# Kernel optimization log

Measured on AMD Instinct MI355X. Metric: run time of the kernel, lower is better.

The kernel has to match this reference:

```python
import jax, jax.numpy as jnp
import numpy as np

N_NODES = 100000
N_EDGES = 1600000
D_IN = 128
D_OUT = 128
EPS = 1e-12  # torch F.normalize default eps


def setup_inputs() -> dict:
    key = jax.random.key(0)
    k1, k2, k3, k4, k5 = jax.random.split(key, 5)
    features = jax.random.normal(k1, (N_NODES, D_IN), dtype=jnp.float32)
    edge_src = jax.random.randint(k2, (N_EDGES,), 0, N_NODES, dtype=jnp.int64)
    edge_dst = jax.random.randint(k3, (N_EDGES,), 0, N_NODES, dtype=jnp.int64)
    node_mask = jnp.ones((N_NODES,), dtype=bool)
    W = jax.random.normal(k4, (D_OUT, D_IN), dtype=jnp.float32) * (1.0 / np.sqrt(D_IN))
    b = jax.random.normal(k5, (D_OUT,), dtype=jnp.float32) * 0.01
    return {"features": features, "edge_src": edge_src, "edge_dst": edge_dst,
            "node_mask": node_mask, "W": W, "b": b}


def reference(features, edge_src, edge_dst, node_mask, W, b):
    # Message passing: sum neighbor (src) features into each dst node.
    msgs = features[edge_src]                                   # [E, D_IN]
    agg = jax.ops.segment_sum(msgs, edge_dst, num_segments=features.shape[0])  # [N, D_IN]
    # Active nodes: h_N[node] = features[node] + sum(neighbors); inactive keep features.
    h_N = jnp.where(node_mask[:, None], features + agg, features)
    # F.normalize(h_N, dim=1): L2 normalize rows with eps clamp.
    norm = jnp.linalg.norm(h_N, axis=1, keepdims=True)
    h_norm = h_N / jnp.maximum(norm, EPS)
    # Linear layer.
    return h_norm @ W.T + b
```

## Files before the change

kernel.cpp:

```cpp
#include <hip/hip_runtime.h>

#define N_NODES 100000
#define D 128
#define N_EDGES 1600000
#define NBINS 391
#define BCAP 8192
#define EPB 4000
#define AST 136
#define LCAP 64

typedef unsigned short u16;
typedef __attribute__((ext_vector_type(8))) short short8;
typedef __attribute__((ext_vector_type(8))) unsigned short ushort8;
typedef __attribute__((ext_vector_type(4))) float f32x4;

__device__ __forceinline__ u16 f2bf(float f) {
    union { float f; unsigned int i; } c;
    c.f = f;
    unsigned int r = c.i + 0x7FFFu + ((c.i >> 16) & 1u);
    return (u16)(r >> 16);
}

__device__ __forceinline__ void bf16_acc8(unsigned int u, float* a) {
    union { unsigned int i; float f; } c;
    c.i = u << 16;          a[0] += c.f;
    c.i = u & 0xffff0000u;  a[1] += c.f;
}

__global__ __launch_bounds__(256) void conv_all(const float* __restrict__ feat,
                                                const float* __restrict__ Wg,
                                                u16* __restrict__ featb,
                                                u16* __restrict__ Wbf,
                                                int* __restrict__ gcnt) {
    const int b = blockIdx.x, t = threadIdx.x;
    if (b < 6250) {
        if (!featb) return;
        int idx = (b * 256 + t) * 8;
        f32x4 v0 = *(const f32x4*)(feat + idx);
        f32x4 v1 = *(const f32x4*)(feat + idx + 4);
        ushort8 o;
        o[0] = f2bf(v0.x); o[1] = f2bf(v0.y); o[2] = f2bf(v0.z); o[3] = f2bf(v0.w);
        o[4] = f2bf(v1.x); o[5] = f2bf(v1.y); o[6] = f2bf(v1.z); o[7] = f2bf(v1.w);
        *(ushort8*)(featb + idx) = o;
    } else if (b < 6258) {
        int idx = ((b - 6250) * 256 + t) * 8;
        f32x4 v0 = *(const f32x4*)(Wg + idx);
        f32x4 v1 = *(const f32x4*)(Wg + idx + 4);
        ushort8 o;
        o[0] = f2bf(v0.x); o[1] = f2bf(v0.y); o[2] = f2bf(v0.z); o[3] = f2bf(v0.w);
        o[4] = f2bf(v1.x); o[5] = f2bf(v1.y); o[6] = f2bf(v1.z); o[7] = f2bf(v1.w);
        *(ushort8*)(Wbf + idx) = o;
    } else {
        gcnt[t] = 0;
        gcnt[t + 256] = 0;
    }
}

__global__ __launch_bounds__(256) void bin_edges(const int* __restrict__ esrc,
                                                 const int* __restrict__ edst,
                                                 int* __restrict__ gcnt,
                                                 unsigned* __restrict__ pool) {
    __shared__ unsigned stash[EPB];
    __shared__ u16 sbin[EPB];
    __shared__ int hist[NBINS];
    __shared__ int hbase[NBINS];
    const int t = threadIdx.x;
    const int base = blockIdx.x * EPB;

    for (int bb = t; bb < NBINS; bb += 256) hist[bb] = 0;
    __syncthreads();
    for (int i = t; i < EPB; i += 256) {
        int s = esrc[base + i];
        int d0 = edst[base + i];
        stash[i] = ((unsigned)(d0 & 255) << 17) | (unsigned)s;
        sbin[i] = (u16)(d0 >> 8);
        atomicAdd(&hist[d0 >> 8], 1);
    }
    __syncthreads();
    for (int bb = t; bb < NBINS; bb += 256) {
        int h = hist[bb];
        hbase[bb] = h ? atomicAdd(gcnt + bb, h) : 0;
        hist[bb] = 0;
    }
    __syncthreads();
    for (int i = t; i < EPB; i += 256) {
        int bb = sbin[i];
        int r  = atomicAdd(&hist[bb], 1);
        int pos = hbase[bb] + r;
        if (pos < BCAP) pool[bb * BCAP + pos] = stash[i];
    }
}

template<bool BF16FEAT>
__global__ __launch_bounds__(256) void fused_gnl(const void* __restrict__ featv,
                                                 const int* __restrict__ gcnt,
                                                 const unsigned* __restrict__ pool,
                                                 const u16* __restrict__ Wbf,
                                                 const float* __restrict__ bg,
                                                 float* __restrict__ out) {
    __shared__ u16 Al[32 * AST];
    __shared__ int lists[32 * LCAP];
    __shared__ int lcnt[32];
    const int t = threadIdx.x;
    const int nbase = blockIdx.x * 32;
    const int nl = t >> 3;
    const int g = t & 7;
    const int n = nbase + nl;

    {
        const int bin = blockIdx.x >> 3;
        const unsigned sub = (unsigned)(blockIdx.x & 7) << 5;
        int ne = gcnt[bin];
        if (ne > BCAP) ne = BCAP;
        if (t < 32) lcnt[t] = 0;
        __syncthreads();
        const unsigned* seg = pool + bin * BCAP;
        for (int i = t; i < ne; i += 256) {
            unsigned p = seg[i];
            unsigned rel = (p >> 17) - sub;
            if (rel < 32u) {
                int r = atomicAdd(&lcnt[rel], 1);
                if (r < LCAP) lists[rel * LCAP + r] = (int)(p & 0x1FFFFu);
            }
        }
        __syncthreads();
    }

    float acc[16];
    if (BF16FEAT) {
        const u16* fb = (const u16*)featv + (size_t)n * D + g * 16;
        uint4 p0 = *(const uint4*)(fb);
        uint4 p1 = *(const uint4*)(fb + 8);
        #pragma unroll
        for (int k = 0; k < 16; k++) acc[k] = 0.f;
        bf16_acc8(p0.x, acc + 0);  bf16_acc8(p0.y, acc + 2);
        bf16_acc8(p0.z, acc + 4);  bf16_acc8(p0.w, acc + 6);
        bf16_acc8(p1.x, acc + 8);  bf16_acc8(p1.y, acc + 10);
        bf16_acc8(p1.z, acc + 12); bf16_acc8(p1.w, acc + 14);
    } else {
        const float* ff = (const float*)featv + (size_t)n * D + g * 16;
        f32x4 v0 = *(const f32x4*)(ff);
        f32x4 v1 = *(const f32x4*)(ff + 4);
        f32x4 v2 = *(const f32x4*)(ff + 8);
        f32x4 v3 = *(const f32x4*)(ff + 12);
        acc[0]=v0.x; acc[1]=v0.y; acc[2]=v0.z; acc[3]=v0.w;
        acc[4]=v1.x; acc[5]=v1.y; acc[6]=v1.z; acc[7]=v1.w;
        acc[8]=v2.x; acc[9]=v2.y; acc[10]=v2.z; acc[11]=v2.w;
        acc[12]=v3.x; acc[13]=v3.y; acc[14]=v3.z; acc[15]=v3.w;
    }

    int deg = lcnt[nl];
    if (deg > LCAP) deg = LCAP;
    const int* bk = lists + nl * LCAP;
    int e = 0;
    if (BF16FEAT) {
        const u16* fb = (const u16*)featv;
        for (; e + 4 <= deg; e += 4) {
            int4 s4 = *(const int4*)(bk + e);
            const u16* r0 = fb + (size_t)s4.x * D + g * 16;
            const u16* r1 = fb + (size_t)s4.y * D + g * 16;
            const u16* r2 = fb + (size_t)s4.z * D + g * 16;
            const u16* r3 = fb + (size_t)s4.w * D + g * 16;
            uint4 a0 = *(const uint4*)(r0), b0 = *(const uint4*)(r0 + 8);
            uint4 a1 = *(const uint4*)(r1), b1 = *(const uint4*)(r1 + 8);
            uint4 a2 = *(const uint4*)(r2), b2 = *(const uint4*)(r2 + 8);
            uint4 a3 = *(const uint4*)(r3), b3 = *(const uint4*)(r3 + 8);
            bf16_acc8(a0.x, acc+0); bf16_acc8(a0.y, acc+2); bf16_acc8(a0.z, acc+4); bf16_acc8(a0.w, acc+6);
            bf16_acc8(b0.x, acc+8); bf16_acc8(b0.y, acc+10); bf16_acc8(b0.z, acc+12); bf16_acc8(b0.w, acc+14);
            bf16_acc8(a1.x, acc+0); bf16_acc8(a1.y, acc+2); bf16_acc8(a1.z, acc+4); bf16_acc8(a1.w, acc+6);
            bf16_acc8(b1.x, acc+8); bf16_acc8(b1.y, acc+10); bf16_acc8(b1.z, acc+12); bf16_acc8(b1.w, acc+14);
            bf16_acc8(a2.x, acc+0); bf16_acc8(a2.y, acc+2); bf16_acc8(a2.z, acc+4); bf16_acc8(a2.w, acc+6);
            bf16_acc8(b2.x, acc+8); bf16_acc8(b2.y, acc+10); bf16_acc8(b2.z, acc+12); bf16_acc8(b2.w, acc+14);
            bf16_acc8(a3.x, acc+0); bf16_acc8(a3.y, acc+2); bf16_acc8(a3.z, acc+4); bf16_acc8(a3.w, acc+6);
            bf16_acc8(b3.x, acc+8); bf16_acc8(b3.y, acc+10); bf16_acc8(b3.z, acc+12); bf16_acc8(b3.w, acc+14);
        }
        for (; e < deg; e++) {
            const u16* r0 = fb + (size_t)bk[e] * D + g * 16;
            uint4 a0 = *(const uint4*)(r0), b0 = *(const uint4*)(r0 + 8);
            bf16_acc8(a0.x, acc+0); bf16_acc8(a0.y, acc+2); bf16_acc8(a0.z, acc+4); bf16_acc8(a0.w, acc+6);
            bf16_acc8(b0.x, acc+8); bf16_acc8(b0.y, acc+10); bf16_acc8(b0.z, acc+12); bf16_acc8(b0.w, acc+14);
        }
    } else {
        const float* ff = (const float*)featv;
        for (; e + 2 <= deg; e += 2) {
            int2 s2 = *(const int2*)(bk + e);
            const float* r0 = ff + (size_t)s2.x * D + g * 16;
            const float* r1 = ff + (size_t)s2.y * D + g * 16;
            f32x4 x0 = *(const f32x4*)(r0),     x1 = *(const f32x4*)(r0 + 4);
            f32x4 x2 = *(const f32x4*)(r0 + 8), x3 = *(const f32x4*)(r0 + 12);
            f32x4 y0 = *(const f32x4*)(r1),     y1 = *(const f32x4*)(r1 + 4);
            f32x4 y2 = *(const f32x4*)(r1 + 8), y3 = *(const f32x4*)(r1 + 12);
            acc[0]+=x0.x+y0.x; acc[1]+=x0.y+y0.y; acc[2]+=x0.z+y0.z; acc[3]+=x0.w+y0.w;
            acc[4]+=x1.x+y1.x; acc[5]+=x1.y+y1.y; acc[6]+=x1.z+y1.z; acc[7]+=x1.w+y1.w;
            acc[8]+=x2.x+y2.x; acc[9]+=x2.y+y2.y; acc[10]+=x2.z+y2.z; acc[11]+=x2.w+y2.w;
            acc[12]+=x3.x+y3.x; acc[13]+=x3.y+y3.y; acc[14]+=x3.z+y3.z; acc[15]+=x3.w+y3.w;
        }
        for (; e < deg; e++) {
            const float* r0 = ff + (size_t)bk[e] * D + g * 16;
            f32x4 x0 = *(const f32x4*)(r0),     x1 = *(const f32x4*)(r0 + 4);
            f32x4 x2 = *(const f32x4*)(r0 + 8), x3 = *(const f32x4*)(r0 + 12);
            acc[0]+=x0.x; acc[1]+=x0.y; acc[2]+=x0.z; acc[3]+=x0.w;
            acc[4]+=x1.x; acc[5]+=x1.y; acc[6]+=x1.z; acc[7]+=x1.w;
            acc[8]+=x2.x; acc[9]+=x2.y; acc[10]+=x2.z; acc[11]+=x2.w;
            acc[12]+=x3.x; acc[13]+=x3.y; acc[14]+=x3.z; acc[15]+=x3.w;
        }
    }

    float ss = 0.f;
    #pragma unroll
    for (int k = 0; k < 16; k++) ss += acc[k] * acc[k];
    #pragma unroll
    for (int off = 4; off; off >>= 1) ss += __shfl_xor(ss, off, 8);
    const float inv = 1.0f / fmaxf(sqrtf(ss), 1e-12f);

    {
        ushort8 o0, o1;
        o0[0]=f2bf(acc[0]*inv); o0[1]=f2bf(acc[1]*inv); o0[2]=f2bf(acc[2]*inv); o0[3]=f2bf(acc[3]*inv);
        o0[4]=f2bf(acc[4]*inv); o0[5]=f2bf(acc[5]*inv); o0[6]=f2bf(acc[6]*inv); o0[7]=f2bf(acc[7]*inv);
        o1[0]=f2bf(acc[8]*inv); o1[1]=f2bf(acc[9]*inv); o1[2]=f2bf(acc[10]*inv); o1[3]=f2bf(acc[11]*inv);
        o1[4]=f2bf(acc[12]*inv); o1[5]=f2bf(acc[13]*inv); o1[6]=f2bf(acc[14]*inv); o1[7]=f2bf(acc[15]*inv);
        u16* dst = Al + nl * AST + g * 16;
        *(ushort8*)(dst)     = o0;
        *(ushort8*)(dst + 8) = o1;
    }
    __syncthreads();

    const int w = t >> 6, lane = t & 63;
    const int mb = (w >> 1) * 16, nb = (w & 1) * 64;
    const int quad = lane >> 4, r = lane & 15;
    f32x4 c0 = {0,0,0,0}, c1 = {0,0,0,0}, c2 = {0,0,0,0}, c3 = {0,0,0,0};
    #pragma unroll
    for (int kt = 0; kt < 4; kt++) {
        const int ko = kt * 32 + quad * 8;
        short8 a  = *(const short8*)(Al + (mb + r) * AST + ko);
        short8 b0 = *(const short8*)(Wbf + (nb +  0 + r) * D + ko);
        short8 b1 = *(const short8*)(Wbf + (nb + 16 + r) * D + ko);
        short8 b2 = *(const short8*)(Wbf + (nb + 32 + r) * D + ko);
        short8 b3 = *(const short8*)(Wbf + (nb + 48 + r) * D + ko);
        c0 = __builtin_amdgcn_mfma_f32_16x16x32_bf16(a, b0, c0, 0, 0, 0);
        c1 = __builtin_amdgcn_mfma_f32_16x16x32_bf16(a, b1, c1, 0, 0, 0);
        c2 = __builtin_amdgcn_mfma_f32_16x16x32_bf16(a, b2, c2, 0, 0, 0);
        c3 = __builtin_amdgcn_mfma_f32_16x16x32_bf16(a, b3, c3, 0, 0, 0);
    }

    {
        const float bb0 = bg[nb + r], bb1 = bg[nb + 16 + r];
        const float bb2 = bg[nb + 32 + r], bb3 = bg[nb + 48 + r];
        float* outb = out + (size_t)(nbase + mb + quad * 4) * D;
        #pragma unroll
        for (int reg = 0; reg < 4; reg++) {
            float* rowp = outb + reg * D + nb + r;
            rowp[0]  = c0[reg] + bb0;
            rowp[16] = c1[reg] + bb1;
            rowp[32] = c2[reg] + bb2;
            rowp[48] = c3[reg] + bb3;
        }
    }
}

__global__ __launch_bounds__(256) void scatter(const float* __restrict__ feat,
                                               const int* __restrict__ esrc,
                                               const int* __restrict__ edst,
                                               float* __restrict__ agg) {
    int gid = blockIdx.x * 256 + threadIdx.x;
    int e = gid >> 5;
    int q = (gid & 31) << 2;
    int s = esrc[e];
    int d0 = edst[e];
    const float4 a = *(const float4*)(feat + s * D + q);
    float* dst = agg + d0 * D + q;
    unsafeAtomicAdd(dst + 0, a.x);
    unsafeAtomicAdd(dst + 1, a.y);
    unsafeAtomicAdd(dst + 2, a.z);
    unsafeAtomicAdd(dst + 3, a.w);
}

__global__ __launch_bounds__(256) void norm_linear_mfma(const float* __restrict__ Wg,
                                                        const float* __restrict__ bg,
                                                        float* __restrict__ out) {
    __shared__ u16 Wl[128 * AST];
    __shared__ u16 Al[32 * AST];
    __shared__ float bl[128];
    const int t = threadIdx.x;
    const int nbase = blockIdx.x * 32;

    for (int idx = t * 8; idx < 128 * 128; idx += 256 * 8) {
        int row = idx >> 7, col = idx & 127;
        f32x4 v0 = *(const f32x4*)(Wg + idx);
        f32x4 v1 = *(const f32x4*)(Wg + idx + 4);
        u16* dst = Wl + row * AST + col;
        dst[0] = f2bf(v0.x); dst[1] = f2bf(v0.y); dst[2] = f2bf(v0.z); dst[3] = f2bf(v0.w);
        dst[4] = f2bf(v1.x); dst[5] = f2bf(v1.y); dst[6] = f2bf(v1.z); dst[7] = f2bf(v1.w);
    }
    if (t < 128) bl[t] = bg[t];
    {
        const int n = t >> 3, seg = t & 7;
        const float* src = out + (nbase + n) * D + seg * 16;
        f32x4 v0 = *(const f32x4*)(src);
        f32x4 v1 = *(const f32x4*)(src + 4);
        f32x4 v2 = *(const f32x4*)(src + 8);
        f32x4 v3 = *(const f32x4*)(src + 12);
        float ss = v0.x*v0.x + v0.y*v0.y + v0.z*v0.z + v0.w*v0.w
                 + v1.x*v1.x + v1.y*v1.y + v1.z*v1.z + v1.w*v1.w
                 + v2.x*v2.x + v2.y*v2.y + v2.z*v2.z + v2.w*v2.w
                 + v3.x*v3.x + v3.y*v3.y + v3.z*v3.z + v3.w*v3.w;
        #pragma unroll
        for (int off = 4; off; off >>= 1) ss += __shfl_xor(ss, off, 8);
        const float inv = 1.0f / fmaxf(sqrtf(ss), 1e-12f);
        u16* dst = Al + n * AST + seg * 16;
        dst[0]  = f2bf(v0.x * inv); dst[1]  = f2bf(v0.y * inv);
        dst[2]  = f2bf(v0.z * inv); dst[3]  = f2bf(v0.w * inv);
        dst[4]  = f2bf(v1.x * inv); dst[5]  = f2bf(v1.y * inv);
        dst[6]  = f2bf(v1.z * inv); dst[7]  = f2bf(v1.w * inv);
        dst[8]  = f2bf(v2.x * inv); dst[9]  = f2bf(v2.y * inv);
        dst[10] = f2bf(v2.z * inv); dst[11] = f2bf(v2.w * inv);
        dst[12] = f2bf(v3.x * inv); dst[13] = f2bf(v3.y * inv);
        dst[14] = f2bf(v3.z * inv); dst[15] = f2bf(v3.w * inv);
    }
    __syncthreads();

    const int w = t >> 6, lane = t & 63;
    const int mb = (w >> 1) * 16, nb = (w & 1) * 64;
    const int quad = lane >> 4, r = lane & 15;
    f32x4 c0 = {0,0,0,0}, c1 = {0,0,0,0}, c2 = {0,0,0,0}, c3 = {0,0,0,0};
    #pragma unroll
    for (int kt = 0; kt < 4; kt++) {
        const int ko = kt * 32 + quad * 8;
        short8 a = *(const short8*)(Al + (mb + r) * AST + ko);
        short8 b0 = *(const short8*)(Wl + (nb +  0 + r) * AST + ko);
        short8 b1 = *(const short8*)(Wl + (nb + 16 + r) * AST + ko);
        short8 b2 = *(const short8*)(Wl + (nb + 32 + r) * AST + ko);
        short8 b3 = *(const short8*)(Wl + (nb + 48 + r) * AST + ko);
        c0 = __builtin_amdgcn_mfma_f32_16x16x32_bf16(a, b0, c0, 0, 0, 0);
        c1 = __builtin_amdgcn_mfma_f32_16x16x32_bf16(a, b1, c1, 0, 0, 0);
        c2 = __builtin_amdgcn_mfma_f32_16x16x32_bf16(a, b2, c2, 0, 0, 0);
        c3 = __builtin_amdgcn_mfma_f32_16x16x32_bf16(a, b3, c3, 0, 0, 0);
    }
    {
        float* outb = out + (nbase + mb + quad * 4) * D;
        const float bb0 = bl[nb + r], bb1 = bl[nb + 16 + r];
        const float bb2 = bl[nb + 32 + r], bb3 = bl[nb + 48 + r];
        #pragma unroll
        for (int reg = 0; reg < 4; reg++) {
            float* rowp = outb + reg * D + nb + r;
            rowp[0]  = c0[reg] + bb0;
            rowp[16] = c1[reg] + bb1;
            rowp[32] = c2[reg] + bb2;
            rowp[48] = c3[reg] + bb3;
        }
    }
}

extern "C" void kernel_launch(void* const* d_in, const int* in_sizes, int n_in,
                              void* d_out, int out_size, void* d_ws, size_t ws_size,
                              hipStream_t stream) {
    const float* feat = (const float*)d_in[0];
    const int*   esrc = (const int*)d_in[1];
    const int*   edst = (const int*)d_in[2];
    const float* W = (const float*)d_in[n_in - 2];
    const float* b = (const float*)d_in[n_in - 1];
    float* out = (float*)d_out;

    const long poolw = (long)NBINS * BCAP;
    const long need_f32  = 512 + 8192 + poolw;
    const long need_bf16 = need_f32 + 6400000;
    const long availw = (long)(ws_size / 4);

    if (availw >= need_f32) {
        const bool bf16feat = (availw >= need_bf16);
        int* gcnt = (int*)d_ws;
        u16* Wbf = (u16*)(gcnt + 512);
        unsigned* pool = (unsigned*)(Wbf + 16384);
        u16* featb = bf16feat ? (u16*)(pool + poolw) : (u16*)nullptr;

        conv_all<<<6259, 256, 0, stream>>>(feat, W, featb, Wbf, gcnt);
        bin_edges<<<N_EDGES / EPB, 256, 0, stream>>>(esrc, edst, gcnt, pool);
        if (bf16feat)
            fused_gnl<true><<<3125, 256, 0, stream>>>(featb, gcnt, pool, Wbf, b, out);
        else
            fused_gnl<false><<<3125, 256, 0, stream>>>(feat, gcnt, pool, Wbf, b, out);
    } else {
        hipMemcpyAsync(out, feat, (size_t)N_NODES * D * sizeof(float),
                       hipMemcpyDeviceToDevice, stream);
        scatter<<<(N_EDGES * 32) / 256, 256, 0, stream>>>(feat, esrc, edst, out);
        norm_linear_mfma<<<N_NODES / 32, 256, 0, stream>>>(W, b, out);
    }
}
```

Measured before the change: 223.2 us.

## Bin edges per 32-node block with direct global atomics instead of two-level binning

Replaces the shared-memory histogram binning kernel (391 coarse bins of 256 nodes) with a simple per-edge kernel that atomically appends each edge into one of 3125 bins matching the 32-node blocks of the fused kernel. Each fused block now scans only its own bin, not a 256-node bin it has to filter, which removes the redundant 8x scanning. The per-node lists in LDS are padded to stride 68 to reduce bank conflicts. The cost is 1.6M global atomics on contended counters, whose ordering is nondeterministic, plus a bin capacity of 1024 edges that silently drops overflow.

```diff
diff --git a/kernel.cpp b/kernel.cpp
--- a/kernel.cpp
+++ b/kernel.cpp
@@ -3,11 +3,11 @@
 #define N_NODES 100000
 #define D 128
 #define N_EDGES 1600000
-#define NBINS 391
-#define BCAP 8192
-#define EPB 4000
+#define NBINS 3125
+#define BCAP 1024
 #define AST 136
 #define LCAP 64
+#define LST 68
 
 typedef unsigned short u16;
 typedef __attribute__((ext_vector_type(8))) short short8;
@@ -51,44 +51,21 @@
         o[4] = f2bf(v1.x); o[5] = f2bf(v1.y); o[6] = f2bf(v1.z); o[7] = f2bf(v1.w);
         *(ushort8*)(Wbf + idx) = o;
     } else {
-        gcnt[t] = 0;
-        gcnt[t + 256] = 0;
-    }
-}
-
-__global__ __launch_bounds__(256) void bin_edges(const int* __restrict__ esrc,
-                                                 const int* __restrict__ edst,
-                                                 int* __restrict__ gcnt,
-                                                 unsigned* __restrict__ pool) {
-    __shared__ unsigned stash[EPB];
-    __shared__ u16 sbin[EPB];
-    __shared__ int hist[NBINS];
-    __shared__ int hbase[NBINS];
-    const int t = threadIdx.x;
-    const int base = blockIdx.x * EPB;
-
-    for (int bb = t; bb < NBINS; bb += 256) hist[bb] = 0;
-    __syncthreads();
-    for (int i = t; i < EPB; i += 256) {
-        int s = esrc[base + i];
-        int d0 = edst[base + i];
-        stash[i] = ((unsigned)(d0 & 255) << 17) | (unsigned)s;
-        sbin[i] = (u16)(d0 >> 8);
-        atomicAdd(&hist[d0 >> 8], 1);
-    }
-    __syncthreads();
-    for (int bb = t; bb < NBINS; bb += 256) {
-        int h = hist[bb];
-        hbase[bb] = h ? atomicAdd(gcnt + bb, h) : 0;
-        hist[bb] = 0;
-    }
-    __syncthreads();
-    for (int i = t; i < EPB; i += 256) {
-        int bb = sbin[i];
-        int r  = atomicAdd(&hist[bb], 1);
-        int pos = hbase[bb] + r;
-        if (pos < BCAP) pool[bb * BCAP + pos] = stash[i];
-    }
+        int i = (b - 6258) * 256 + t;
+        if (i < 3328) gcnt[i] = 0;
+    }
+}
+
+__global__ __launch_bounds__(256) void place_bins(const int* __restrict__ esrc,
+                                                  const int* __restrict__ edst,
+                                                  int* __restrict__ gcnt,
+                                                  unsigned* __restrict__ pool) {
+    const int e = blockIdx.x * 256 + threadIdx.x;
+    int s = esrc[e];
+    int d0 = edst[e];
+    int bin = d0 >> 5;
+    int pos = atomicAdd(&gcnt[bin], 1);
+    if (pos < BCAP) pool[bin * BCAP + pos] = ((unsigned)(d0 & 31) << 17) | (unsigned)s;
 }
 
 template<bool BF16FEAT>
@@ -99,7 +76,7 @@
                                                  const float* __restrict__ bg,
                                                  float* __restrict__ out) {
     __shared__ u16 Al[32 * AST];
-    __shared__ int lists[32 * LCAP];
+    __shared__ int lists[32 * LST];
     __shared__ int lcnt[32];
     const int t = threadIdx.x;
     const int nbase = blockIdx.x * 32;
@@ -108,20 +85,16 @@
     const int n = nbase + nl;
 
     {
-        const int bin = blockIdx.x >> 3;
-        const unsigned sub = (unsigned)(blockIdx.x & 7) << 5;
-        int ne = gcnt[bin];
+        int ne = gcnt[blockIdx.x];
         if (ne > BCAP) ne = BCAP;
         if (t < 32) lcnt[t] = 0;
         __syncthreads();
-        const unsigned* seg = pool + bin * BCAP;
+        const unsigned* seg = pool + blockIdx.x * BCAP;
         for (int i = t; i < ne; i += 256) {
             unsigned p = seg[i];
-            unsigned rel = (p >> 17) - sub;
-            if (rel < 32u) {
-                int r = atomicAdd(&lcnt[rel], 1);
-                if (r < LCAP) lists[rel * LCAP + r] = (int)(p & 0x1FFFFu);
-            }
+            unsigned rel = p >> 17;
+            int r = atomicAdd(&lcnt[rel], 1);
+            if (r < LCAP) lists[rel * LST + r] = (int)(p & 0x1FFFFu);
         }
         __syncthreads();
     }
@@ -151,7 +124,7 @@
 
     int deg = lcnt[nl];
     if (deg > LCAP) deg = LCAP;
-    const int* bk = lists + nl * LCAP;
+    const int* bk = lists + nl * LST;
     int e = 0;
     if (BF16FEAT) {
         const u16* fb = (const u16*)featv;
@@ -362,23 +335,23 @@
     float* out = (float*)d_out;
 
     const long poolw = (long)NBINS * BCAP;
-    const long need_f32  = 512 + 8192 + poolw;
+    const long need_f32  = 3328 + 8192 + poolw;
     const long need_bf16 = need_f32 + 6400000;
     const long availw = (long)(ws_size / 4);
 
     if (availw >= need_f32) {
         const bool bf16feat = (availw >= need_bf16);
         int* gcnt = (int*)d_ws;
-        u16* Wbf = (u16*)(gcnt + 512);
+        u16* Wbf = (u16*)(gcnt + 3328);
         unsigned* pool = (unsigned*)(Wbf + 16384);
         u16* featb = bf16feat ? (u16*)(pool + poolw) : (u16*)nullptr;
 
-        conv_all<<<6259, 256, 0, stream>>>(feat, W, featb, Wbf, gcnt);
-        bin_edges<<<N_EDGES / EPB, 256, 0, stream>>>(esrc, edst, gcnt, pool);
+        conv_all<<<6271, 256, 0, stream>>>(feat, W, featb, Wbf, gcnt);
+        place_bins<<<N_EDGES / 256, 256, 0, stream>>>(esrc, edst, gcnt, pool);
         if (bf16feat)
-            fused_gnl<true><<<3125, 256, 0, stream>>>(featb, gcnt, pool, Wbf, b, out);
+            fused_gnl<true><<<NBINS, 256, 0, stream>>>(featb, gcnt, pool, Wbf, b, out);
         else
-            fused_gnl<false><<<3125, 256, 0, stream>>>(feat, gcnt, pool, Wbf, b, out);
+            fused_gnl<false><<<NBINS, 256, 0, stream>>>(feat, gcnt, pool, Wbf, b, out);
     } else {
         hipMemcpyAsync(out, feat, (size_t)N_NODES * D * sizeof(float),
                        hipMemcpyDeviceToDevice, stream);
```

After: 323.1 us. +44.8%, slower.

## Fuse edge binning with bf16 conversion into one prep kernel and sort bins locally

Applied to the files above, without the earlier changes.

Merges the feature/weight bf16 conversion and the edge binning into a single prep launch so the two independent stages can run side by side, and moves the counter zeroing to a memset. The binning now counting-sorts edges by bin in shared memory before writing, so global pool writes are contiguous per bin. It also shrinks the per-bin capacity, which reduces the pool footprint but risks dropping edges if a bin overflows, and pads the per-node neighbor lists to a stride of 68 to avoid LDS bank conflicts. The conversion part becomes a grid-stride loop over fewer blocks.

```diff
diff --git a/kernel.cpp b/kernel.cpp
--- a/kernel.cpp
+++ b/kernel.cpp
@@ -4,10 +4,14 @@
 #define D 128
 #define N_EDGES 1600000
 #define NBINS 391
-#define BCAP 8192
+#define BCAP 4608
 #define EPB 4000
+#define NBB 400
+#define NCVB 2048
+#define NV ((N_NODES * D) / 8)
 #define AST 136
 #define LCAP 64
+#define LST 68
 
 typedef unsigned short u16;
 typedef __attribute__((ext_vector_type(8))) short short8;
@@ -27,67 +31,73 @@
     c.i = u & 0xffff0000u;  a[1] += c.f;
 }
 
-__global__ __launch_bounds__(256) void conv_all(const float* __restrict__ feat,
-                                                const float* __restrict__ Wg,
-                                                u16* __restrict__ featb,
-                                                u16* __restrict__ Wbf,
-                                                int* __restrict__ gcnt) {
+__global__ __launch_bounds__(256) void prep(const float* __restrict__ feat,
+                                            const float* __restrict__ Wg,
+                                            const int* __restrict__ esrc,
+                                            const int* __restrict__ edst,
+                                            u16* __restrict__ featb,
+                                            u16* __restrict__ Wbf,
+                                            int* __restrict__ gcnt,
+                                            unsigned* __restrict__ pool) {
     const int b = blockIdx.x, t = threadIdx.x;
-    if (b < 6250) {
+    if (b < NBB) {
+        __shared__ unsigned sorted[EPB];
+        __shared__ u16 sbin[EPB];
+        __shared__ int hist[NBINS];
+        __shared__ int hbase[NBINS];
+        __shared__ int loff[NBINS];
+        const int base = b * EPB;
+
+        for (int i = t; i < NBINS; i += 256) hist[i] = 0;
+        __syncthreads();
+        for (int i = t; i < EPB; i += 256)
+            atomicAdd(&hist[edst[base + i] >> 8], 1);
+        __syncthreads();
+        if (t == 0) {
+            int run = 0;
+            for (int c = 0; c < NBINS; c++) { loff[c] = run; run += hist[c]; }
+        }
+        __syncthreads();
+        for (int i = t; i < NBINS; i += 256) {
+            int h = hist[i];
+            hbase[i] = h ? atomicAdd(gcnt + i, h) : 0;
+            hist[i] = 0;
+        }
+        __syncthreads();
+        for (int i = t; i < EPB; i += 256) {
+            int s = esrc[base + i];
+            int d0 = edst[base + i];
+            int bb = d0 >> 8;
+            int r = atomicAdd(&hist[bb], 1);
+            int slot = loff[bb] + r;
+            sorted[slot] = ((unsigned)(d0 & 255) << 17) | (unsigned)s;
+            sbin[slot] = (u16)bb;
+        }
+        __syncthreads();
+        for (int i = t; i < EPB; i += 256) {
+            int bb = sbin[i];
+            int pos = hbase[bb] + (i - loff[bb]);
+            if (pos < BCAP) pool[bb * BCAP + pos] = sorted[i];
+        }
+    } else if (b < NBB + NCVB) {
         if (!featb) return;
-        int idx = (b * 256 + t) * 8;
-        f32x4 v0 = *(const f32x4*)(feat + idx);
-        f32x4 v1 = *(const f32x4*)(feat + idx + 4);
-        ushort8 o;
-        o[0] = f2bf(v0.x); o[1] = f2bf(v0.y); o[2] = f2bf(v0.z); o[3] = f2bf(v0.w);
-        o[4] = f2bf(v1.x); o[5] = f2bf(v1.y); o[6] = f2bf(v1.z); o[7] = f2bf(v1.w);
-        *(ushort8*)(featb + idx) = o;
-    } else if (b < 6258) {
-        int idx = ((b - 6250) * 256 + t) * 8;
+        for (int i = (b - NBB) * 256 + t; i < NV; i += NCVB * 256) {
+            int idx = i * 8;
+            f32x4 v0 = *(const f32x4*)(feat + idx);
+            f32x4 v1 = *(const f32x4*)(feat + idx + 4);
+            ushort8 o;
+            o[0] = f2bf(v0.x); o[1] = f2bf(v0.y); o[2] = f2bf(v0.z); o[3] = f2bf(v0.w);
+            o[4] = f2bf(v1.x); o[5] = f2bf(v1.y); o[6] = f2bf(v1.z); o[7] = f2bf(v1.w);
+            *(ushort8*)(featb + idx) = o;
+        }
+    } else {
+        int idx = ((b - NBB - NCVB) * 256 + t) * 8;
         f32x4 v0 = *(const f32x4*)(Wg + idx);
         f32x4 v1 = *(const f32x4*)(Wg + idx + 4);
         ushort8 o;
         o[0] = f2bf(v0.x); o[1] = f2bf(v0.y); o[2] = f2bf(v0.z); o[3] = f2bf(v0.w);
         o[4] = f2bf(v1.x); o[5] = f2bf(v1.y); o[6] = f2bf(v1.z); o[7] = f2bf(v1.w);
         *(ushort8*)(Wbf + idx) = o;
-    } else {
-        gcnt[t] = 0;
-        gcnt[t + 256] = 0;
-    }
-}
-
-__global__ __launch_bounds__(256) void bin_edges(const int* __restrict__ esrc,
-                                                 const int* __restrict__ edst,
-                                                 int* __restrict__ gcnt,
-                                                 unsigned* __restrict__ pool) {
-    __shared__ unsigned stash[EPB];
-    __shared__ u16 sbin[EPB];
-    __shared__ int hist[NBINS];
-    __shared__ int hbase[NBINS];
-    const int t = threadIdx.x;
-    const int base = blockIdx.x * EPB;
-
-    for (int bb = t; bb < NBINS; bb += 256) hist[bb] = 0;
-    __syncthreads();
-    for (int i = t; i < EPB; i += 256) {
-        int s = esrc[base + i];
-        int d0 = edst[base + i];
-        stash[i] = ((unsigned)(d0 & 255) << 17) | (unsigned)s;
-        sbin[i] = (u16)(d0 >> 8);
-        atomicAdd(&hist[d0 >> 8], 1);
-    }
-    __syncthreads();
-    for (int bb = t; bb < NBINS; bb += 256) {
-        int h = hist[bb];
-        hbase[bb] = h ? atomicAdd(gcnt + bb, h) : 0;
-        hist[bb] = 0;
-    }
-    __syncthreads();
-    for (int i = t; i < EPB; i += 256) {
-        int bb = sbin[i];
-        int r  = atomicAdd(&hist[bb], 1);
-        int pos = hbase[bb] + r;
-        if (pos < BCAP) pool[bb * BCAP + pos] = stash[i];
     }
 }
 
@@ -99,7 +109,7 @@
                                                  const float* __restrict__ bg,
                                                  float* __restrict__ out) {
     __shared__ u16 Al[32 * AST];
-    __shared__ int lists[32 * LCAP];
+    __shared__ int lists[32 * LST];
     __shared__ int lcnt[32];
     const int t = threadIdx.x;
     const int nbase = blockIdx.x * 32;
@@ -114,13 +124,13 @@
         if (ne > BCAP) ne = BCAP;
         if (t < 32) lcnt[t] = 0;
         __syncthreads();
-        const unsigned* seg = pool + bin * BCAP;
+        const unsigned* seg = pool + (size_t)bin * BCAP;
         for (int i = t; i < ne; i += 256) {
             unsigned p = seg[i];
             unsigned rel = (p >> 17) - sub;
             if (rel < 32u) {
                 int r = atomicAdd(&lcnt[rel], 1);
-                if (r < LCAP) lists[rel * LCAP + r] = (int)(p & 0x1FFFFu);
+                if (r < LCAP) lists[rel * LST + r] = (int)(p & 0x1FFFFu);
             }
         }
         __syncthreads();
@@ -151,7 +161,7 @@
 
     int deg = lcnt[nl];
     if (deg > LCAP) deg = LCAP;
-    const int* bk = lists + nl * LCAP;
+    const int* bk = lists + nl * LST;
     int e = 0;
     if (BF16FEAT) {
         const u16* fb = (const u16*)featv;
@@ -373,12 +383,12 @@
         unsigned* pool = (unsigned*)(Wbf + 16384);
         u16* featb = bf16feat ? (u16*)(pool + poolw) : (u16*)nullptr;
 
-        conv_all<<<6259, 256, 0, stream>>>(feat, W, featb, Wbf, gcnt);
-        bin_edges<<<N_EDGES / EPB, 256, 0, stream>>>(esrc, edst, gcnt, pool);
+        hipMemsetAsync(gcnt, 0, 512 * sizeof(int), stream);
+        prep<<<NBB + NCVB + 8, 256, 0, stream>>>(feat, W, esrc, edst, featb, Wbf, gcnt, pool);
         if (bf16feat)
-            fused_gnl<true><<<3125, 256, 0, stream>>>(featb, gcnt, pool, Wbf, b, out);
+            fused_gnl<true><<<N_NODES / 32, 256, 0, stream>>>(featb, gcnt, pool, Wbf, b, out);
         else
-            fused_gnl<false><<<3125, 256, 0, stream>>>(feat, gcnt, pool, Wbf, b, out);
+            fused_gnl<false><<<N_NODES / 32, 256, 0, stream>>>(feat, gcnt, pool, Wbf, b, out);
     } else {
         hipMemcpyAsync(out, feat, (size_t)N_NODES * D * sizeof(float),
                        hipMemcpyDeviceToDevice, stream);
```

After: 225.8 us. No clear change (+1.2%).
